# Kernel optimization log

Hardware: AMD Instinct MI355X
Metric: run time of the kernel (lower is better)

The kernel has to match this reference:

```python
import jax, jax.numpy as jnp
import numpy as np

B, H, S, DK = 4, 16, 4096, 64


def setup_inputs() -> dict:
    key = jax.random.key(0)
    kq, kk, kv = jax.random.split(key, 3)
    Q = jax.random.normal(kq, (B, H, S, DK), dtype=jnp.float32)
    K = jax.random.normal(kk, (B, H, S, DK), dtype=jnp.float32)
    V = jax.random.normal(kv, (B, H, S, DK), dtype=jnp.float32)
    return {"Q": Q, "K": K, "V": V}


def reference(Q, K, V):
    d_k = K.shape[-1]
    inv_sqrt_dk = jnp.sqrt(jnp.float32(1.0) / d_k)
    # [B, H, S, S] materialized scores (faithful to the naive original)
    scores = jnp.einsum('bhqd,bhkd->bhqk', Q, K) * inv_sqrt_dk
    # causal mask: original subtracts (1 - tril) * 1e9 from scores
    s_q, s_k = Q.shape[-2], K.shape[-2]
    causal = jnp.tril(jnp.ones((s_q, s_k), dtype=jnp.float32))
    scores = scores - (1.0 - causal) * 1e9
    probs = jax.nn.softmax(scores, axis=-1)
    out = jnp.einsum('bhqk,bhkd->bhqd', probs, V)
    return out
```

## Files before the change

kernel.cpp:

```cpp
#include <hip/hip_runtime.h>
#include <hip/hip_bf16.h>

typedef short bf16x8 __attribute__((ext_vector_type(8)));
typedef float f32x16 __attribute__((ext_vector_type(16)));
typedef float f32x4v __attribute__((ext_vector_type(4)));

static constexpr int SEQ = 4096;
static constexpr int HD  = 64;
static constexpr int BQ  = 128;
static constexpr int BK  = 64;
static constexpr float QSCALE = 0.125f * 1.44269504088896340736f;

union F8 { bf16x8 v; unsigned short u[8]; uint4 q; };

__device__ __forceinline__ unsigned short f2bf(float x) {
    __bf16 b = (__bf16)x;
    return __builtin_bit_cast(unsigned short, b);
}
__device__ __forceinline__ unsigned pk2(float lo, float hi) {
    return (unsigned)f2bf(lo) | ((unsigned)f2bf(hi) << 16);
}
__device__ __forceinline__ float exp2fast(float x) {
    return __builtin_amdgcn_exp2f(x);
}

__device__ __forceinline__ int kperm_src(int rho) {
    return (rho & 0x23) | (((rho >> 3) & 1) << 4) |
           (((rho >> 2) & 1) << 3) | (((rho >> 4) & 1) << 2);
}
__device__ __forceinline__ int kperm_dst(int src) {
    return (src & 0x23) | (((src >> 2) & 1) << 4) |
           (((src >> 4) & 1) << 3) | (((src >> 3) & 1) << 2);
}

__global__ __launch_bounds__(256)
void prep_kv(const float* __restrict__ K, const float* __restrict__ V,
             unsigned short* __restrict__ ws)
{
    __shared__ float vt[64][68];

    const int tid = threadIdx.x;
    const int bid = blockIdx.x;
    const size_t sbase = ((size_t)(bid >> 6)) * (SEQ * HD) +
                         ((size_t)(bid & 63)) * (64 * HD);
    unsigned short* Kt = ws + (size_t)bid * 4096;
    unsigned short* Vt = ws + (size_t)16777216 + (size_t)bid * 4096;

    #pragma unroll
    for (int i = 0; i < 2; ++i) {
        const int c   = tid + 256 * i;
        const int row = c >> 3, j = c & 7;
        const int jsrc = j ^ (row & 7);
        const float* src = K + sbase + kperm_src(row) * HD + 8 * jsrc;
        float4 a = *(const float4*)src;
        float4 b = *(const float4*)(src + 4);
        *(uint4*)(Kt + row * 64 + 8 * j) =
            make_uint4(pk2(a.x, a.y), pk2(a.z, a.w), pk2(b.x, b.y), pk2(b.z, b.w));
    }

    {
        const int r  = tid >> 2;
        const int cb = (tid & 3) << 4;
        const float* src = V + sbase + r * HD + cb;
        *(float4*)&vt[r][cb + 0]  = *(const float4*)(src);
        *(float4*)&vt[r][cb + 4]  = *(const float4*)(src + 4);
        *(float4*)&vt[r][cb + 8]  = *(const float4*)(src + 8);
        *(float4*)&vt[r][cb + 12] = *(const float4*)(src + 12);
    }
    __syncthreads();
    #pragma unroll
    for (int i = 0; i < 2; ++i) {
        const int c = tid + 256 * i;
        const int d = c >> 3, j = c & 7;
        const int kb = 8 * (j ^ (d & 7));
        unsigned u[4];
        #pragma unroll
        for (int p = 0; p < 4; ++p)
            u[p] = pk2(vt[kb + 2 * p][d], vt[kb + 2 * p + 1][d]);
        *(uint4*)(Vt + d * 64 + 8 * j) = make_uint4(u[0], u[1], u[2], u[3]);
    }
}

template<bool PRE>
__global__ __launch_bounds__(256, 4)
void mha_fwd(const float* __restrict__ Q, const float* __restrict__ K,
             const float* __restrict__ V, float* __restrict__ O,
             const unsigned short* __restrict__ ws)
{
    __shared__ unsigned short Kl[2][4096];
    __shared__ unsigned short Vl[2][4096];

    const int tid  = threadIdx.x;
    const int lane = tid & 63;
    const int w    = tid >> 6;
    const int l31  = lane & 31;
    const int h    = lane >> 5;

    const int bid = blockIdx.x;
    const int bh  = bid & 63;
    const int qb  = 31 - (bid >> 6);
    const int q0  = qb * BQ;
    const size_t base = (size_t)bh * (SEQ * HD);

    const int qlane  = q0 + 32 * w + l31;
    const int qmax_w = q0 + 32 * w + 31;

    bf16x8 qf[4];
    {
        const float* qrow = Q + base + (size_t)qlane * HD;
        #pragma unroll
        for (int c = 0; c < 4; ++c) {
            const f32x4v x = *(const f32x4v*)(qrow + 16 * c + 8 * h);
            const f32x4v y = *(const f32x4v*)(qrow + 16 * c + 8 * h + 4);
            F8 f;
            #pragma unroll
            for (int j = 0; j < 4; ++j) f.u[j]     = f2bf(x[j] * QSCALE);
            #pragma unroll
            for (int j = 0; j < 4; ++j) f.u[4 + j] = f2bf(y[j] * QSCALE);
            qf[c] = f.v;
        }
    }

    F8 onesf;
    #pragma unroll
    for (int j = 0; j < 8; ++j) onesf.u[j] = 0x3F80;

    f32x16 oacc[2];
    f32x16 lacc;
    f32x16 zacc;
    #pragma unroll
    for (int r = 0; r < 16; ++r) {
        oacc[0][r] = 0.f; oacc[1][r] = 0.f; lacc[r] = 0.f; zacc[r] = 0.f;
    }

    const int nkt = 2 * qb + 2;

    const int ksr = tid >> 2;
    const int ksc = (tid & 3) << 4;
    const int vkb = tid >> 4;
    const int vdb = tid & 15;

    f32x4v kreg[4], vreg[4];

    const unsigned short* Kws = ws;
    const unsigned short* Vws = ws + (size_t)16777216;

    auto stage_pre = [&](int buf, int kt) {
        const size_t toff = (((size_t)bh << 6) + (size_t)kt) << 12;
        #pragma unroll
        for (int i = 0; i < 2; ++i) {
            const int ch = 2 * w + i;
            const unsigned short* kg = Kws + toff + ch * 512 + lane * 8;
            const unsigned short* vg = Vws + toff + ch * 512 + lane * 8;
            __builtin_amdgcn_global_load_lds(
                (const __attribute__((address_space(1))) void*)(const void*)kg,
                (__attribute__((address_space(3))) void*)(void*)&Kl[buf][ch * 512],
                16, 0, 0);
            __builtin_amdgcn_global_load_lds(
                (const __attribute__((address_space(1))) void*)(const void*)vg,
                (__attribute__((address_space(3))) void*)(void*)&Vl[buf][ch * 512],
                16, 0, 0);
        }
    };

    auto load_regs = [&](int kt) {
        const int k0 = kt * BK;
        const float* ks = K + base + (size_t)(k0 + ksr) * HD + ksc;
        kreg[0] = *(const f32x4v*)(ks);
        kreg[1] = *(const f32x4v*)(ks + 4);
        kreg[2] = *(const f32x4v*)(ks + 8);
        kreg[3] = *(const f32x4v*)(ks + 12);
        const float* vs = V + base + (size_t)(k0 + 4 * vkb) * HD + 4 * vdb;
        vreg[0] = *(const f32x4v*)(vs);
        vreg[1] = *(const f32x4v*)(vs + HD);
        vreg[2] = *(const f32x4v*)(vs + 2 * HD);
        vreg[3] = *(const f32x4v*)(vs + 3 * HD);
    };

    auto write_lds = [&](int buf) {
        unsigned u[8];
        #pragma unroll
        for (int i = 0; i < 4; ++i) {
            u[2*i]   = pk2(kreg[i][0], kreg[i][1]);
            u[2*i+1] = pk2(kreg[i][2], kreg[i][3]);
        }
        const int drow = kperm_dst(ksr);
        char* kd = (char*)&Kl[buf][0] + drow * 128;
        const int o0 = (2 * ksc) ^ ((drow & 7) << 4);
        *(uint4*)(kd + o0)        = make_uint4(u[0], u[1], u[2], u[3]);
        *(uint4*)(kd + (o0 ^ 16)) = make_uint4(u[4], u[5], u[6], u[7]);
        #pragma unroll
        for (int i = 0; i < 4; ++i) {
            const int c = (i + (vdb >> 1)) & 3;
            const int d = 4 * vdb + c;
            const unsigned lo = pk2(vreg[0][c], vreg[1][c]);
            const unsigned hi = pk2(vreg[2][c], vreg[3][c]);
            char* vd = (char*)&Vl[buf][0] + d * 128 + ((8 * vkb) ^ ((d & 7) << 4));
            *(uint2*)vd = make_uint2(lo, hi);
        }
    };

    if constexpr (PRE) { stage_pre(0, 0); }
    else               { load_regs(0); write_lds(0); }
    __syncthreads();

    for (int kt = 0; kt < nkt; ++kt) {
        const int cur = kt & 1;
        const bool hn = (kt + 1) < nkt;
        if constexpr (PRE) { if (hn) stage_pre(cur ^ 1, kt + 1); }
        else               { if (hn) load_regs(kt + 1); }

        if (64 * kt <= qmax_w) {
            const unsigned short* Kb = &Kl[cur][0];
            const unsigned short* Vb = &Vl[cur][0];
            const int k0 = kt * BK;

            f32x16 sacc[2];
            #pragma unroll
            for (int s = 0; s < 2; ++s) {
                const int row = 32 * s + l31;
                const char* rp = (const char*)Kb + row * 128;
                const int sw = (row & 7) << 4;
                __builtin_amdgcn_s_setprio(1);
                #pragma unroll
                for (int c = 0; c < 4; ++c) {
                    bf16x8 kf = *(const bf16x8*)(rp + ((32 * c + 16 * h) ^ sw));
                    sacc[s] = __builtin_amdgcn_mfma_f32_32x32x16_bf16(
                        kf, qf[c], c == 0 ? zacc : sacc[s], 0, 0, 0);
                }
                __builtin_amdgcn_s_setprio(0);
            }

            if (kt >= nkt - 2) {
                #pragma unroll
                for (int s = 0; s < 2; ++s)
                    #pragma unroll
                    for (int r = 0; r < 16; ++r) {
                        const int key = k0 + 32 * s + 16 * ((r >> 2) & 1) +
                                        4 * ((r >> 3) & 1) + 8 * h + (r & 3);
                        if (key > qlane) sacc[s][r] = -1e30f;
                    }
            }

            #pragma unroll
            for (int s = 0; s < 2; ++s) {
                #pragma unroll
                for (int r = 0; r < 16; ++r) sacc[s][r] = exp2fast(sacc[s][r]);

                #pragma unroll
                for (int m0 = 0; m0 < 2; ++m0) {
                    const int kc = 2 * s + m0;
                    F8 pf;
                    pf.q.x = pk2(sacc[s][4 * m0 + 0],  sacc[s][4 * m0 + 1]);
                    pf.q.y = pk2(sacc[s][4 * m0 + 2],  sacc[s][4 * m0 + 3]);
                    pf.q.z = pk2(sacc[s][8 + 4 * m0 + 0], sacc[s][8 + 4 * m0 + 1]);
                    pf.q.w = pk2(sacc[s][8 + 4 * m0 + 2], sacc[s][8 + 4 * m0 + 3]);
                    __builtin_amdgcn_s_setprio(1);
                    lacc = __builtin_amdgcn_mfma_f32_32x32x16_bf16(onesf.v, pf.v, lacc, 0, 0, 0);
                    #pragma unroll
                    for (int dsi = 0; dsi < 2; ++dsi) {
                        const int row = 32 * dsi + l31;
                        const char* vp = (const char*)Vb + row * 128 +
                                         ((32 * kc + 16 * h) ^ ((row & 7) << 4));
                        bf16x8 vf = *(const bf16x8*)vp;
                        oacc[dsi] = __builtin_amdgcn_mfma_f32_32x32x16_bf16(vf, pf.v, oacc[dsi], 0, 0, 0);
                    }
                    __builtin_amdgcn_s_setprio(0);
                }
            }
        }

        if constexpr (!PRE) { if (hn) write_lds(cur ^ 1); }
        __syncthreads();
    }

    const float il = 1.0f / lacc[0];
    float* orow = O + base + (size_t)qlane * HD;
    #pragma unroll
    for (int dsi = 0; dsi < 2; ++dsi)
        #pragma unroll
        for (int g = 0; g < 4; ++g) {
            f32x4v o4;
            #pragma unroll
            for (int j = 0; j < 4; ++j) o4[j] = oacc[dsi][4 * g + j] * il;
            *(f32x4v*)(orow + 32 * dsi + 8 * g + 4 * h) = o4;
        }
}

extern "C" void kernel_launch(void* const* d_in, const int* in_sizes, int n_in,
                              void* d_out, int out_size, void* d_ws, size_t ws_size,
                              hipStream_t stream) {
    const float* Q = (const float*)d_in[0];
    const float* K = (const float*)d_in[1];
    const float* V = (const float*)d_in[2];
    float* O = (float*)d_out;
    (void)in_sizes; (void)n_in; (void)out_size;

    const size_t need = (size_t)2 * 16777216 * sizeof(unsigned short);
    if (ws_size >= need) {
        unsigned short* ws = (unsigned short*)d_ws;
        prep_kv<<<dim3(64 * 64), 256, 0, stream>>>(K, V, ws);
        mha_fwd<true><<<dim3(32 * 64), 256, 0, stream>>>(Q, K, V, O, ws);
    } else {
        mha_fwd<false><<<dim3(32 * 64), 256, 0, stream>>>(Q, K, V, O, nullptr);
    }
}
```

Baseline: 209.0 us.

## Double key tile to 128 in workspace attention kernel with unified LDS buffer

Result: slower. 255.5 us (+22.3%).

```diff
diff --git a/kernel.cpp b/kernel.cpp
--- a/kernel.cpp
+++ b/kernel.cpp
@@ -8,7 +8,6 @@
 static constexpr int SEQ = 4096;
 static constexpr int HD  = 64;
 static constexpr int BQ  = 128;
-static constexpr int BK  = 64;
 static constexpr float QSCALE = 0.125f * 1.44269504088896340736f;
 
 union F8 { bf16x8 v; unsigned short u[8]; uint4 q; };
@@ -81,14 +80,11 @@
     }
 }
 
-template<bool PRE>
-__global__ __launch_bounds__(256, 4)
-void mha_fwd(const float* __restrict__ Q, const float* __restrict__ K,
-             const float* __restrict__ V, float* __restrict__ O,
-             const unsigned short* __restrict__ ws)
+__global__ __launch_bounds__(256, 2)
+void mha_fwd2(const float* __restrict__ Q, float* __restrict__ O,
+              const unsigned short* __restrict__ ws)
 {
-    __shared__ unsigned short Kl[2][4096];
-    __shared__ unsigned short Vl[2][4096];
+    __shared__ __align__(16) unsigned short LDSu[32768];
 
     const int tid  = threadIdx.x;
     const int lane = tid & 63;
@@ -102,8 +98,7 @@
     const int q0  = qb * BQ;
     const size_t base = (size_t)bh * (SEQ * HD);
 
-    const int qlane  = q0 + 32 * w + l31;
-    const int qmax_w = q0 + 32 * w + 31;
+    const int qlane = q0 + 32 * w + l31;
 
     bf16x8 qf[4];
     {
@@ -133,6 +128,168 @@
         oacc[0][r] = 0.f; oacc[1][r] = 0.f; lacc[r] = 0.f; zacc[r] = 0.f;
     }
 
+    const int nkt2 = qb + 1;
+
+    char* lds0 = (char*)&LDSu[0];
+    const int sw = (l31 & 7) << 4;
+    char* a4[4];
+    #pragma unroll
+    for (int c = 0; c < 4; ++c)
+        a4[c] = lds0 + l31 * 128 + (((c << 5) | (h << 4)) ^ sw);
+
+    const unsigned short* Kws = ws;
+    const unsigned short* Vws = ws + (size_t)16777216;
+
+    auto stage = [&](int buf, int kt2) {
+        const size_t toff = (((size_t)bh << 6) + ((size_t)kt2 << 1)) << 12;
+        const int bufoff = buf << 14;
+        #pragma unroll
+        for (int i = 0; i < 4; ++i) {
+            const int ch = 4 * w + i;
+            const unsigned short* kg = Kws + toff + ch * 512 + lane * 8;
+            const unsigned short* vg = Vws + toff + ch * 512 + lane * 8;
+            __builtin_amdgcn_global_load_lds(
+                (const __attribute__((address_space(1))) void*)(const void*)kg,
+                (__attribute__((address_space(3))) void*)(void*)(lds0 + bufoff + ch * 1024),
+                16, 0, 0);
+            __builtin_amdgcn_global_load_lds(
+                (const __attribute__((address_space(1))) void*)(const void*)vg,
+                (__attribute__((address_space(3))) void*)(void*)(lds0 + 32768 + bufoff + ch * 1024),
+                16, 0, 0);
+        }
+    };
+
+    stage(0, 0);
+    __syncthreads();
+
+    for (int kt2 = 0; kt2 < nkt2; ++kt2) {
+        const bool hn = (kt2 + 1) < nkt2;
+        if (hn) stage((kt2 & 1) ^ 1, kt2 + 1);
+
+        const int k0 = kt2 * 128;
+
+        f32x16 sacc[4];
+        #pragma unroll
+        for (int s = 0; s < 4; ++s) {
+            const int t = s >> 1, u = s & 1;
+            __builtin_amdgcn_s_setprio(1);
+            #pragma unroll
+            for (int c = 0; c < 4; ++c) {
+                bf16x8 kf = *(const bf16x8*)(a4[c] + t * 8192 + u * 4096);
+                sacc[s] = __builtin_amdgcn_mfma_f32_32x32x16_bf16(
+                    kf, qf[c], c == 0 ? zacc : sacc[s], 0, 0, 0);
+            }
+            __builtin_amdgcn_s_setprio(0);
+        }
+
+        if (kt2 == nkt2 - 1) {
+            #pragma unroll
+            for (int s = 0; s < 4; ++s)
+                #pragma unroll
+                for (int r = 0; r < 16; ++r) {
+                    const int key = k0 + 64 * (s >> 1) + 32 * (s & 1) +
+                                    16 * ((r >> 2) & 1) + 4 * ((r >> 3) & 1) +
+                                    8 * h + (r & 3);
+                    if (key > qlane) sacc[s][r] = -1e30f;
+                }
+        }
+
+        #pragma unroll
+        for (int kc = 0; kc < 8; ++kc) {
+            const int s = kc >> 1, m0 = kc & 1;
+            const int t = kc >> 2, kcl = kc & 3;
+            float e0 = exp2fast(sacc[s][4 * m0 + 0]);
+            float e1 = exp2fast(sacc[s][4 * m0 + 1]);
+            float e2 = exp2fast(sacc[s][4 * m0 + 2]);
+            float e3 = exp2fast(sacc[s][4 * m0 + 3]);
+            float e4 = exp2fast(sacc[s][8 + 4 * m0 + 0]);
+            float e5 = exp2fast(sacc[s][8 + 4 * m0 + 1]);
+            float e6 = exp2fast(sacc[s][8 + 4 * m0 + 2]);
+            float e7 = exp2fast(sacc[s][8 + 4 * m0 + 3]);
+            F8 pf;
+            pf.q.x = pk2(e0, e1);
+            pf.q.y = pk2(e2, e3);
+            pf.q.z = pk2(e4, e5);
+            pf.q.w = pk2(e6, e7);
+            __builtin_amdgcn_s_setprio(1);
+            lacc = __builtin_amdgcn_mfma_f32_32x32x16_bf16(onesf.v, pf.v, lacc, 0, 0, 0);
+            {
+                bf16x8 vf0 = *(const bf16x8*)(a4[kcl] + 32768 + t * 8192 + 0 * 4096);
+                oacc[0] = __builtin_amdgcn_mfma_f32_32x32x16_bf16(vf0, pf.v, oacc[0], 0, 0, 0);
+                bf16x8 vf1 = *(const bf16x8*)(a4[kcl] + 32768 + t * 8192 + 1 * 4096);
+                oacc[1] = __builtin_amdgcn_mfma_f32_32x32x16_bf16(vf1, pf.v, oacc[1], 0, 0, 0);
+            }
+            __builtin_amdgcn_s_setprio(0);
+        }
+
+        #pragma unroll
+        for (int c = 0; c < 4; ++c)
+            a4[c] = (char*)((size_t)a4[c] ^ 16384);
+
+        __syncthreads();
+    }
+
+    const float il = 1.0f / lacc[0];
+    float* orow = O + base + (size_t)qlane * HD;
+    #pragma unroll
+    for (int dsi = 0; dsi < 2; ++dsi)
+        #pragma unroll
+        for (int g = 0; g < 4; ++g) {
+            f32x4v o4;
+            #pragma unroll
+            for (int j = 0; j < 4; ++j) o4[j] = oacc[dsi][4 * g + j] * il;
+            *(f32x4v*)(orow + 32 * dsi + 8 * g + 4 * h) = o4;
+        }
+}
+
+__global__ __launch_bounds__(256, 4)
+void mha_fwd_fb(const float* __restrict__ Q, const float* __restrict__ K,
+                const float* __restrict__ V, float* __restrict__ O)
+{
+    __shared__ unsigned short Kl[2][4096];
+    __shared__ unsigned short Vl[2][4096];
+
+    const int tid  = threadIdx.x;
+    const int lane = tid & 63;
+    const int w    = tid >> 6;
+    const int l31  = lane & 31;
+    const int h    = lane >> 5;
+
+    const int bid = blockIdx.x;
+    const int bh  = bid & 63;
+    const int qb  = 31 - (bid >> 6);
+    const int q0  = qb * BQ;
+    const size_t base = (size_t)bh * (SEQ * HD);
+
+    const int qlane  = q0 + 32 * w + l31;
+    const int qmax_w = q0 + 32 * w + 31;
+
+    bf16x8 qf[4];
+    {
+        const float* qrow = Q + base + (size_t)qlane * HD;
+        #pragma unroll
+        for (int c = 0; c < 4; ++c) {
+            const f32x4v x = *(const f32x4v*)(qrow + 16 * c + 8 * h);
+            const f32x4v y = *(const f32x4v*)(qrow + 16 * c + 8 * h + 4);
+            F8 f;
+            #pragma unroll
+            for (int j = 0; j < 4; ++j) f.u[j]     = f2bf(x[j] * QSCALE);
+            #pragma unroll
+            for (int j = 0; j < 4; ++j) f.u[4 + j] = f2bf(y[j] * QSCALE);
+            qf[c] = f.v;
+        }
+    }
+
+    F8 onesf;
+    #pragma unroll
+    for (int j = 0; j < 8; ++j) onesf.u[j] = 0x3F80;
+
+    f32x16 oacc[2], lacc, zacc;
+    #pragma unroll
+    for (int r = 0; r < 16; ++r) {
+        oacc[0][r] = 0.f; oacc[1][r] = 0.f; lacc[r] = 0.f; zacc[r] = 0.f;
+    }
+
     const int nkt = 2 * qb + 2;
 
     const int ksr = tid >> 2;
@@ -142,29 +299,8 @@
 
     f32x4v kreg[4], vreg[4];
 
-    const unsigned short* Kws = ws;
-    const unsigned short* Vws = ws + (size_t)16777216;
-
-    auto stage_pre = [&](int buf, int kt) {
-        const size_t toff = (((size_t)bh << 6) + (size_t)kt) << 12;
-        #pragma unroll
-        for (int i = 0; i < 2; ++i) {
-            const int ch = 2 * w + i;
-            const unsigned short* kg = Kws + toff + ch * 512 + lane * 8;
-            const unsigned short* vg = Vws + toff + ch * 512 + lane * 8;
-            __builtin_amdgcn_global_load_lds(
-                (const __attribute__((address_space(1))) void*)(const void*)kg,
-                (__attribute__((address_space(3))) void*)(void*)&Kl[buf][ch * 512],
-                16, 0, 0);
-            __builtin_amdgcn_global_load_lds(
-                (const __attribute__((address_space(1))) void*)(const void*)vg,
-                (__attribute__((address_space(3))) void*)(void*)&Vl[buf][ch * 512],
-                16, 0, 0);
-        }
-    };
-
     auto load_regs = [&](int kt) {
-        const int k0 = kt * BK;
+        const int k0 = kt * 64;
         const float* ks = K + base + (size_t)(k0 + ksr) * HD + ksc;
         kreg[0] = *(const f32x4v*)(ks);
         kreg[1] = *(const f32x4v*)(ks + 4);
@@ -200,35 +336,31 @@
         }
     };
 
-    if constexpr (PRE) { stage_pre(0, 0); }
-    else               { load_regs(0); write_lds(0); }
+    load_regs(0); write_lds(0);
     __syncthreads();
 
     for (int kt = 0; kt < nkt; ++kt) {
         const int cur = kt & 1;
         const bool hn = (kt + 1) < nkt;
-        if constexpr (PRE) { if (hn) stage_pre(cur ^ 1, kt + 1); }
-        else               { if (hn) load_regs(kt + 1); }
+        if (hn) load_regs(kt + 1);
 
         if (64 * kt <= qmax_w) {
             const unsigned short* Kb = &Kl[cur][0];
             const unsigned short* Vb = &Vl[cur][0];
-            const int k0 = kt * BK;
+            const int k0 = kt * 64;
 
             f32x16 sacc[2];
             #pragma unroll
             for (int s = 0; s < 2; ++s) {
                 const int row = 32 * s + l31;
                 const char* rp = (const char*)Kb + row * 128;
-                const int sw = (row & 7) << 4;
-                __builtin_amdgcn_s_setprio(1);
+                const int swl = (row & 7) << 4;
                 #pragma unroll
                 for (int c = 0; c < 4; ++c) {
-                    bf16x8 kf = *(const bf16x8*)(rp + ((32 * c + 16 * h) ^ sw));
+                    bf16x8 kf = *(const bf16x8*)(rp + ((32 * c + 16 * h) ^ swl));
                     sacc[s] = __builtin_amdgcn_mfma_f32_32x32x16_bf16(
                         kf, qf[c], c == 0 ? zacc : sacc[s], 0, 0, 0);
                 }
-                __builtin_amdgcn_s_setprio(0);
             }
 
             if (kt >= nkt - 2) {
@@ -246,7 +378,6 @@
             for (int s = 0; s < 2; ++s) {
                 #pragma unroll
                 for (int r = 0; r < 16; ++r) sacc[s][r] = exp2fast(sacc[s][r]);
-
                 #pragma unroll
                 for (int m0 = 0; m0 < 2; ++m0) {
                     const int kc = 2 * s + m0;
@@ -255,7 +386,6 @@
                     pf.q.y = pk2(sacc[s][4 * m0 + 2],  sacc[s][4 * m0 + 3]);
                     pf.q.z = pk2(sacc[s][8 + 4 * m0 + 0], sacc[s][8 + 4 * m0 + 1]);
                     pf.q.w = pk2(sacc[s][8 + 4 * m0 + 2], sacc[s][8 + 4 * m0 + 3]);
-                    __builtin_amdgcn_s_setprio(1);
                     lacc = __builtin_amdgcn_mfma_f32_32x32x16_bf16(onesf.v, pf.v, lacc, 0, 0, 0);
                     #pragma unroll
                     for (int dsi = 0; dsi < 2; ++dsi) {
@@ -265,12 +395,11 @@
                         bf16x8 vf = *(const bf16x8*)vp;
                         oacc[dsi] = __builtin_amdgcn_mfma_f32_32x32x16_bf16(vf, pf.v, oacc[dsi], 0, 0, 0);
                     }
-                    __builtin_amdgcn_s_setprio(0);
                 }
             }
         }
 
-        if constexpr (!PRE) { if (hn) write_lds(cur ^ 1); }
+        if (hn) write_lds(cur ^ 1);
         __syncthreads();
     }
 
@@ -300,8 +429,8 @@
     if (ws_size >= need) {
         unsigned short* ws = (unsigned short*)d_ws;
         prep_kv<<<dim3(64 * 64), 256, 0, stream>>>(K, V, ws);
-        mha_fwd<true><<<dim3(32 * 64), 256, 0, stream>>>(Q, K, V, O, ws);
+        mha_fwd2<<<dim3(32 * 64), 256, 0, stream>>>(Q, O, ws);
     } else {
-        mha_fwd<false><<<dim3(32 * 64), 256, 0, stream>>>(Q, K, V, O, nullptr);
-    }
-}
+        mha_fwd_fb<<<dim3(32 * 64), 256, 0, stream>>>(Q, K, V, O);
+    }
+}
```
